# Kernel tuning notes

Measured on AMD Instinct MI355X. Metric: run time of the kernel, lower is better.

## Reference

```python
import jax, jax.numpy as jnp
import numpy as np

N_NODES = 100000
N_EDGES = 1600000
D_FEAT = 128
HIDDEN = 256


def setup_inputs() -> dict:
    key = jax.random.key(0)
    k1, k2, k3, k4, k5, k6, k7 = jax.random.split(key, 7)
    h = jax.random.normal(k1, (N_NODES, D_FEAT), dtype=jnp.float32)
    src = jax.random.randint(k2, (N_EDGES,), 0, N_NODES, dtype=jnp.int64)
    dst = jax.random.randint(k3, (N_EDGES,), 0, N_NODES, dtype=jnp.int64)
    # Linear weights, torch layout: W [out, in], b [out]
    lim1 = 1.0 / np.sqrt(2 * D_FEAT)
    W1_w = jax.random.uniform(k4, (HIDDEN, 2 * D_FEAT), minval=-lim1, maxval=lim1, dtype=jnp.float32)
    W1_b = jax.random.uniform(k5, (HIDDEN,), minval=-lim1, maxval=lim1, dtype=jnp.float32)
    lim2 = 1.0 / np.sqrt(HIDDEN)
    W2_w = jax.random.uniform(k6, (1, HIDDEN), minval=-lim2, maxval=lim2, dtype=jnp.float32)
    W2_b = jax.random.uniform(k7, (1,), minval=-lim2, maxval=lim2, dtype=jnp.float32)
    return {"h": h, "src": src, "dst": dst, "W1_w": W1_w, "W1_b": W1_b, "W2_w": W2_w, "W2_b": W2_b}


def reference(h, src, dst, W1_w, W1_b, W2_w, W2_b):
    # gather per-edge src/dst node features and concat: [E, 2D]
    x = jnp.concatenate([h[src], h[dst]], axis=1)
    # Linear -> ReLU -> Linear, squeeze last dim -> [E]
    hid = jax.nn.relu(x @ W1_w.T + W1_b)          # [E, H]
    score = (hid @ W2_w.T + W2_b)[:, 0]           # [E]
    return score
```

## Files before the change

### kernel.cpp

```cpp
#include <hip/hip_runtime.h>


#define NNODES 100000
#define E_TOTAL 1600000
#define D 128
#define K2 256
#define H 256

typedef short bf16x8 __attribute__((ext_vector_type(8)));
typedef short bf16x4 __attribute__((ext_vector_type(4)));
typedef float f32x4 __attribute__((ext_vector_type(4)));
typedef const __attribute__((address_space(1))) unsigned short* gas_t;
typedef __attribute__((address_space(3))) unsigned short* las_t;

__device__ __forceinline__ unsigned short f2bf(float f) {
    unsigned u = __float_as_uint(f);
    u += 0x7fff + ((u >> 16) & 1);
    return (unsigned short)(u >> 16);
}
__device__ __forceinline__ float bf2f(unsigned short s) {
    return __uint_as_float((unsigned)s << 16);
}

__global__ void cvt_w1(const float* __restrict__ W1, unsigned short* __restrict__ w1bf, int n4) {
    int i = blockIdx.x * blockDim.x + threadIdx.x;
    if (i >= n4) return;
    float4 v = ((const float4*)W1)[i];
    ushort4 o;
    o.x = f2bf(v.x); o.y = f2bf(v.y); o.z = f2bf(v.z); o.w = f2bf(v.w);
    ((ushort4*)w1bf)[i] = o;
}

__global__ __launch_bounds__(256, 2) void u_gemm(
    const float* __restrict__ h,
    const unsigned short* __restrict__ w1bf,
    const float* __restrict__ b1,
    unsigned short* __restrict__ Us,
    unsigned short* __restrict__ Ud)
{
    __shared__ __align__(16) unsigned short A[64 * 136];
    __shared__ __align__(16) unsigned short S[64 * 268];

    const int tid = threadIdx.x;
    const int wave = tid >> 6;
    const int lane = tid & 63;
    const int l15 = lane & 15;
    const int quad = lane >> 4;

    const int tile = blockIdx.x >> 1;
    const int half = blockIdx.x & 1;
    const int r0 = tile * 64;
    int rows = NNODES - r0; if (rows > 64) rows = 64;
    const int koff = half * 128;
    unsigned short* U = half ? Ud : Us;

    bf16x8 B[4][4];
    float bias[4];
#pragma unroll
    for (int nt = 0; nt < 4; ++nt) {
        const int n = wave * 64 + nt * 16 + l15;
        bias[nt] = half ? 0.f : b1[n];
#pragma unroll
        for (int kit = 0; kit < 4; ++kit)
            B[kit][nt] = *(const bf16x8*)(w1bf + (size_t)n * K2 + koff + kit * 32 + quad * 8);
    }

    const float4* hf4 = (const float4*)(h + (size_t)r0 * D);
    const int lim = rows * 32;
#pragma unroll
    for (int i = 0; i < 8; ++i) {
        int j = tid + i * 256;
        if (j < lim) {
            float4 v = hf4[j];
            bf16x4 b;
            b[0] = (short)f2bf(v.x); b[1] = (short)f2bf(v.y);
            b[2] = (short)f2bf(v.z); b[3] = (short)f2bf(v.w);
            *(bf16x4*)&A[(j >> 5) * 136 + (j & 31) * 4] = b;
        }
    }
    __syncthreads();

    f32x4 acc[4][4];
    const f32x4 zero = {0.f, 0.f, 0.f, 0.f};
#pragma unroll
    for (int ms = 0; ms < 4; ++ms)
#pragma unroll
        for (int nt = 0; nt < 4; ++nt)
            acc[ms][nt] = zero;

#pragma unroll
    for (int kit = 0; kit < 4; ++kit) {
        bf16x8 a[4];
#pragma unroll
        for (int ms = 0; ms < 4; ++ms)
            a[ms] = *(const bf16x8*)&A[(ms * 16 + l15) * 136 + kit * 32 + quad * 8];
#pragma unroll
        for (int ms = 0; ms < 4; ++ms)
#pragma unroll
            for (int nt = 0; nt < 4; ++nt)
                acc[ms][nt] = __builtin_amdgcn_mfma_f32_16x16x32_bf16(
                    a[ms], B[kit][nt], acc[ms][nt], 0, 0, 0);
    }

#pragma unroll
    for (int ms = 0; ms < 4; ++ms)
#pragma unroll
        for (int r = 0; r < 4; ++r) {
            const int m = ms * 16 + quad * 4 + r;
#pragma unroll
            for (int nt = 0; nt < 4; ++nt)
                S[m * 268 + wave * 64 + nt * 16 + l15] =
                    f2bf(acc[ms][nt][r] + bias[nt]);
        }
    __syncthreads();

#pragma unroll
    for (int i = 0; i < 8; ++i) {
        const int j = i * 256 + tid;
        const int row = j >> 5;
        const int cc = j & 31;
        if (row < rows) {
            bf16x8 vv = *(const bf16x8*)&S[row * 268 + cc * 8];
            *(bf16x8*)(U + (size_t)(r0 + row) * H + cc * 8) = vv;
        }
    }
}

__global__ __launch_bounds__(256) void edge_score(
    const unsigned short* __restrict__ Us,
    const unsigned short* __restrict__ Ud,
    const int* __restrict__ srcE,
    const int* __restrict__ dstE,
    const float* __restrict__ w2,
    const float* __restrict__ b2p,
    float* __restrict__ out,
    int grp0, int ngrp)
{
    const int gt = blockIdx.x * 256 + threadIdx.x;
    const int l = gt & 15;
    const int q = gt >> 4;
    const int Q = (gridDim.x * 256) >> 4;

    float w2v[16];
#pragma unroll
    for (int j = 0; j < 16; ++j) w2v[j] = w2[l * 16 + j];
    const float b2 = *b2p;

    for (int g = grp0 + q; g < grp0 + ngrp; g += Q) {
        const int e0 = g * 4;
        const int4 s4 = *(const int4*)(srcE + e0);
        const int4 d4 = *(const int4*)(dstE + e0);
        const int sv[4] = {s4.x, s4.y, s4.z, s4.w};
        const int dv[4] = {d4.x, d4.y, d4.z, d4.w};

        bf16x8 u[4][2], v[4][2];
#pragma unroll
        for (int k = 0; k < 4; ++k) {
            const bf16x8* us = (const bf16x8*)(Us + (size_t)sv[k] * H + l * 16);
            const bf16x8* ud = (const bf16x8*)(Ud + (size_t)dv[k] * H + l * 16);
            u[k][0] = us[0]; u[k][1] = us[1];
            v[k][0] = ud[0]; v[k][1] = ud[1];
        }

        float4 res;
        float* resp = (float*)&res;
#pragma unroll
        for (int k = 0; k < 4; ++k) {
            float acc = 0.f;
#pragma unroll
            for (int j = 0; j < 8; ++j) {
                float hv = bf2f((unsigned short)u[k][0][j]) + bf2f((unsigned short)v[k][0][j]);
                acc = fmaf(fmaxf(hv, 0.f), w2v[j], acc);
            }
#pragma unroll
            for (int j = 0; j < 8; ++j) {
                float hv = bf2f((unsigned short)u[k][1][j]) + bf2f((unsigned short)v[k][1][j]);
                acc = fmaf(fmaxf(hv, 0.f), w2v[j + 8], acc);
            }
            acc += __shfl_xor(acc, 1, 16);
            acc += __shfl_xor(acc, 2, 16);
            acc += __shfl_xor(acc, 4, 16);
            acc += __shfl_xor(acc, 8, 16);
            resp[k] = acc + b2;
        }
        if (l == 0) *(float4*)(out + e0) = res;
    }
}


#define TILE_M 32
#define NTILES (E_TOTAL / TILE_M)
#define GRID 2500

#if defined(__has_attribute)
#if __has_attribute(amdgpu_waves_per_eu)
#define LB __launch_bounds__(256) __attribute__((amdgpu_waves_per_eu(2, 2)))
#else
#define LB __launch_bounds__(256, 2)
#endif
#else
#define LB __launch_bounds__(256, 2)
#endif

__global__ void cvt_kernel(const float* __restrict__ h, const float* __restrict__ w1,
                           unsigned short* __restrict__ hbf, unsigned short* __restrict__ w1bf,
                           int n4h, int n4w) {
    int i = blockIdx.x * blockDim.x + threadIdx.x;
    const float* s; unsigned short* d; int j;
    if (i < n4h) { s = h; d = hbf; j = i; }
    else if (i < n4h + n4w) { s = w1; d = w1bf; j = i - n4h; }
    else return;
    float4 v = ((const float4*)s)[j];
    ushort4 o;
    o.x = f2bf(v.x); o.y = f2bf(v.y); o.z = f2bf(v.z); o.w = f2bf(v.w);
    ((ushort4*)d)[j] = o;
}

__global__ LB void edge_mlp(
    const unsigned short* __restrict__ hbf,
    const int* __restrict__ srcE,
    const int* __restrict__ dstE,
    const unsigned short* __restrict__ w1bf,
    const float* __restrict__ b1,
    const float* __restrict__ w2,
    const float* __restrict__ b2p,
    float* __restrict__ out)
{
    __shared__ __align__(16) unsigned short X[2][TILE_M * K2];
    __shared__ float red[2][TILE_M][5];

    const int tid = threadIdx.x;
    const int wave = tid >> 6;
    const int lane = tid & 63;
    const int lane15 = lane & 15;
    const int quad = lane >> 4;

    bf16x8 B[8][4];
#pragma unroll
    for (int kit = 0; kit < 8; ++kit)
#pragma unroll
        for (int nt = 0; nt < 4; ++nt) {
            int n = wave * 64 + nt * 16 + lane15;
            int k = kit * 32 + quad * 8;
            B[kit][nt] = *(const bf16x8*)(w1bf + n * K2 + k);
        }

    float b1v[4], w2v[4];
#pragma unroll
    for (int nt = 0; nt < 4; ++nt) {
        int n = wave * 64 + nt * 16 + lane15;
        b1v[nt] = b1[n];
        w2v[nt] = w2[n];
    }
    const float b2 = *b2p;

    const int r_off = tid >> 5;
    const int c = (tid & 31) ^ (r_off & 7);
    const int half = c >> 4;
    const int fc = c & 15;
    const int* idx_base = half ? dstE : srcE;
    const int gshort = fc * 8;

    const int t0 = blockIdx.x;
    int inode[4];

#pragma unroll
    for (int it = 0; it < 4; ++it)
        inode[it] = idx_base[t0 * TILE_M + it * 8 + r_off];
#pragma unroll
    for (int it = 0; it < 4; ++it)
        __builtin_amdgcn_global_load_lds(
            (gas_t)(hbf + inode[it] * D + gshort),
            (las_t)(&X[0][0] + it * 2048 + wave * 512), 16, 0, 0);
    {
        const int t1 = t0 + GRID;
#pragma unroll
        for (int it = 0; it < 4; ++it)
            inode[it] = idx_base[t1 * TILE_M + it * 8 + r_off];
    }

    int buf = 0;
    int prev_eb = -1;

    for (int tile = t0; tile < NTILES; tile += GRID) {
        __syncthreads();

        const int nt1 = tile + GRID;
        if (nt1 < NTILES) {
            unsigned short* Xn = &X[buf ^ 1][0];
#pragma unroll
            for (int it = 0; it < 4; ++it)
                __builtin_amdgcn_global_load_lds(
                    (gas_t)(hbf + inode[it] * D + gshort),
                    (las_t)(Xn + it * 2048 + wave * 512), 16, 0, 0);
        }
        const int nt2 = tile + 2 * GRID;
        if (nt2 < NTILES) {
            const int eb2 = nt2 * TILE_M;
#pragma unroll
            for (int it = 0; it < 4; ++it)
                inode[it] = idx_base[eb2 + it * 8 + r_off];
        }
        if (prev_eb >= 0 && tid < TILE_M) {
            float s = b2;
#pragma unroll
            for (int w = 0; w < 4; ++w) s += red[buf ^ 1][tid][w];
            out[prev_eb + tid] = s;
        }

        const unsigned short* Xc = &X[buf][0];
        f32x4 acc[2][4];
        const f32x4 zero = {0.f, 0.f, 0.f, 0.f};
#pragma unroll
        for (int ms = 0; ms < 2; ++ms)
#pragma unroll
            for (int nt = 0; nt < 4; ++nt)
                acc[ms][nt] = zero;

#pragma unroll
        for (int kit = 0; kit < 8; ++kit) {
            const int p8 = (((kit * 4 + quad) ^ (lane15 & 7))) * 8;
            bf16x8 a[2];
#pragma unroll
            for (int ms = 0; ms < 2; ++ms)
                a[ms] = *(const bf16x8*)&Xc[(ms * 16 + lane15) * K2 + p8];
#pragma unroll
            for (int ms = 0; ms < 2; ++ms)
#pragma unroll
                for (int nt = 0; nt < 4; ++nt)
                    acc[ms][nt] = __builtin_amdgcn_mfma_f32_16x16x32_bf16(
                        a[ms], B[kit][nt], acc[ms][nt], 0, 0, 0);
        }

#pragma unroll
        for (int ms = 0; ms < 2; ++ms)
#pragma unroll
            for (int r = 0; r < 4; ++r) {
                float p = 0.f;
#pragma unroll
                for (int nt = 0; nt < 4; ++nt) {
                    float hv = acc[ms][nt][r] + b1v[nt];
                    p = fmaf(fmaxf(hv, 0.f), w2v[nt], p);
                }
                p += __shfl_xor(p, 1, 16);
                p += __shfl_xor(p, 2, 16);
                p += __shfl_xor(p, 4, 16);
                p += __shfl_xor(p, 8, 16);
                if (lane15 == 0) red[buf][ms * 16 + quad * 4 + r][wave] = p;
            }
        prev_eb = tile * TILE_M;
        buf ^= 1;
    }

    __syncthreads();
    if (prev_eb >= 0 && tid < TILE_M) {
        float s = b2;
#pragma unroll
        for (int w = 0; w < 4; ++w) s += red[buf ^ 1][tid][w];
        out[prev_eb + tid] = s;
    }
}


extern "C" void kernel_launch(void* const* d_in, const int* in_sizes, int n_in,
                              void* d_out, int out_size, void* d_ws, size_t ws_size,
                              hipStream_t stream) {
    const float* h    = (const float*)d_in[0];
    const int*   srcE = (const int*)d_in[1];
    const int*   dstE = (const int*)d_in[2];
    const float* W1   = (const float*)d_in[3];
    const float* b1   = (const float*)d_in[4];
    const float* w2   = (const float*)d_in[5];
    const float* b2   = (const float*)d_in[6];
    float* out = (float*)d_out;

    char* ws = (char*)d_ws;
    const size_t offUs   = 0;
    const size_t offUd   = 51200000;
    const size_t offW1bf = 102400000;
    const size_t need    = offW1bf + 131072;

    if (ws_size >= need) {
        unsigned short* Us   = (unsigned short*)(ws + offUs);
        unsigned short* Ud   = (unsigned short*)(ws + offUd);
        unsigned short* w1bf = (unsigned short*)(ws + offW1bf);

        cvt_w1<<<(H * K2 / 4 + 255) / 256, 256, 0, stream>>>(W1, w1bf, H * K2 / 4);
        u_gemm<<<2 * ((NNODES + 63) / 64), 256, 0, stream>>>(h, w1bf, b1, Us, Ud);

        const int NGRP = E_TOTAL / 4;
        const int HALF_G = NGRP / 2;
        edge_score<<<2048, 256, 0, stream>>>(Us, Ud, srcE, dstE, w2, b2, out, 0, HALF_G);
        edge_score<<<2048, 256, 0, stream>>>(Us, Ud, srcE, dstE, w2, b2, out, HALF_G, HALF_G);
    } else {
        unsigned short* hbf  = (unsigned short*)d_ws;
        unsigned short* w1bf = hbf + (size_t)NNODES * D;
        int n4h = NNODES * D / 4;
        int n4w = H * K2 / 4;
        int n4 = n4h + n4w;
        cvt_kernel<<<(n4 + 255) / 256, 256, 0, stream>>>(h, W1, hbf, w1bf, n4h, n4w);
        edge_mlp<<<GRID, 256, 0, stream>>>(hbf, srcE, dstE, w1bf, b1, w2, b2, out);
    }
}
```

Before: 371.6 us.

## Pre-convert h to bf16 and stage it via direct global-to-LDS swizzled loads

Node features are converted to bf16 once by a separate kernel. The node GEMM then streams those bf16 rows straight into LDS with global_load_lds, using an XOR-swizzled layout in place of the padded one, so it no longer loads fp32 and converts in registers. The edge scoring pass is split into four launches instead of two. In exchange this adds a full conversion pass over h and needs more workspace; if the workspace is too small, it falls back to the old fused edge MLP path.

```diff
diff --git a/kernel.cpp b/kernel.cpp
--- a/kernel.cpp
+++ b/kernel.cpp
@@ -20,6 +20,20 @@
 }
 __device__ __forceinline__ float bf2f(unsigned short s) {
     return __uint_as_float((unsigned)s << 16);
+}
+
+__global__ void cvt_kernel(const float* __restrict__ h, const float* __restrict__ w1,
+                           unsigned short* __restrict__ hbf, unsigned short* __restrict__ w1bf,
+                           int n4h, int n4w) {
+    int i = blockIdx.x * blockDim.x + threadIdx.x;
+    const float* s; unsigned short* d; int j;
+    if (i < n4h) { s = h; d = hbf; j = i; }
+    else if (i < n4h + n4w) { s = w1; d = w1bf; j = i - n4h; }
+    else return;
+    float4 v = ((const float4*)s)[j];
+    ushort4 o;
+    o.x = f2bf(v.x); o.y = f2bf(v.y); o.z = f2bf(v.z); o.w = f2bf(v.w);
+    ((ushort4*)d)[j] = o;
 }
 
 __global__ void cvt_w1(const float* __restrict__ W1, unsigned short* __restrict__ w1bf, int n4) {
@@ -31,14 +45,14 @@
     ((ushort4*)w1bf)[i] = o;
 }
 
-__global__ __launch_bounds__(256, 2) void u_gemm(
-    const float* __restrict__ h,
+__global__ __launch_bounds__(256, 2) void u_gemm2(
+    const unsigned short* __restrict__ hbf,
     const unsigned short* __restrict__ w1bf,
     const float* __restrict__ b1,
     unsigned short* __restrict__ Us,
     unsigned short* __restrict__ Ud)
 {
-    __shared__ __align__(16) unsigned short A[64 * 136];
+    __shared__ __align__(16) unsigned short A[64 * 128];
     __shared__ __align__(16) unsigned short S[64 * 268];
 
     const int tid = threadIdx.x;
@@ -54,6 +68,18 @@
     const int koff = half * 128;
     unsigned short* U = half ? Ud : Us;
 
+#pragma unroll
+    for (int it = 0; it < 4; ++it) {
+        const int s = it * 256 + tid;
+        const int r = s >> 4;
+        const int p = s & 15;
+        const int c = p ^ (r & 15);
+        if (r < rows)
+            __builtin_amdgcn_global_load_lds(
+                (gas_t)(hbf + (size_t)(r0 + r) * D + c * 8),
+                (las_t)(A + it * 2048 + wave * 512), 16, 0, 0);
+    }
+
     bf16x8 B[4][4];
     float bias[4];
 #pragma unroll
@@ -65,19 +91,6 @@
             B[kit][nt] = *(const bf16x8*)(w1bf + (size_t)n * K2 + koff + kit * 32 + quad * 8);
     }
 
-    const float4* hf4 = (const float4*)(h + (size_t)r0 * D);
-    const int lim = rows * 32;
-#pragma unroll
-    for (int i = 0; i < 8; ++i) {
-        int j = tid + i * 256;
-        if (j < lim) {
-            float4 v = hf4[j];
-            bf16x4 b;
-            b[0] = (short)f2bf(v.x); b[1] = (short)f2bf(v.y);
-            b[2] = (short)f2bf(v.z); b[3] = (short)f2bf(v.w);
-            *(bf16x4*)&A[(j >> 5) * 136 + (j & 31) * 4] = b;
-        }
-    }
     __syncthreads();
 
     f32x4 acc[4][4];
@@ -92,8 +105,11 @@
     for (int kit = 0; kit < 4; ++kit) {
         bf16x8 a[4];
 #pragma unroll
-        for (int ms = 0; ms < 4; ++ms)
-            a[ms] = *(const bf16x8*)&A[(ms * 16 + l15) * 136 + kit * 32 + quad * 8];
+        for (int ms = 0; ms < 4; ++ms) {
+            const int row = ms * 16 + l15;
+            const int p = (kit * 4 + quad) ^ l15;
+            a[ms] = *(const bf16x8*)&A[row * 128 + p * 8];
+        }
 #pragma unroll
         for (int ms = 0; ms < 4; ++ms)
 #pragma unroll
@@ -202,20 +218,6 @@
 #define LB __launch_bounds__(256, 2)
 #endif
 
-__global__ void cvt_kernel(const float* __restrict__ h, const float* __restrict__ w1,
-                           unsigned short* __restrict__ hbf, unsigned short* __restrict__ w1bf,
-                           int n4h, int n4w) {
-    int i = blockIdx.x * blockDim.x + threadIdx.x;
-    const float* s; unsigned short* d; int j;
-    if (i < n4h) { s = h; d = hbf; j = i; }
-    else if (i < n4h + n4w) { s = w1; d = w1bf; j = i - n4h; }
-    else return;
-    float4 v = ((const float4*)s)[j];
-    ushort4 o;
-    o.x = f2bf(v.x); o.y = f2bf(v.y); o.z = f2bf(v.z); o.w = f2bf(v.w);
-    ((ushort4*)d)[j] = o;
-}
-
 __global__ LB void edge_mlp(
     const unsigned short* __restrict__ hbf,
     const int* __restrict__ srcE,
@@ -377,28 +379,40 @@
     char* ws = (char*)d_ws;
     const size_t offUs   = 0;
     const size_t offUd   = 51200000;
-    const size_t offW1bf = 102400000;
-    const size_t need    = offW1bf + 131072;
-
-    if (ws_size >= need) {
+    const size_t offHbf  = 102400000;
+    const size_t offW1v2 = 128000000;
+    const size_t needV2  = offW1v2 + 131072;
+    const size_t offW1v1 = 102400000;
+    const size_t needV1  = offW1v1 + 131072;
+
+    const int NGRP = E_TOTAL / 4;
+
+    if (ws_size >= needV2) {
         unsigned short* Us   = (unsigned short*)(ws + offUs);
         unsigned short* Ud   = (unsigned short*)(ws + offUd);
-        unsigned short* w1bf = (unsigned short*)(ws + offW1bf);
-
-        cvt_w1<<<(H * K2 / 4 + 255) / 256, 256, 0, stream>>>(W1, w1bf, H * K2 / 4);
-        u_gemm<<<2 * ((NNODES + 63) / 64), 256, 0, stream>>>(h, w1bf, b1, Us, Ud);
-
-        const int NGRP = E_TOTAL / 4;
-        const int HALF_G = NGRP / 2;
-        edge_score<<<2048, 256, 0, stream>>>(Us, Ud, srcE, dstE, w2, b2, out, 0, HALF_G);
-        edge_score<<<2048, 256, 0, stream>>>(Us, Ud, srcE, dstE, w2, b2, out, HALF_G, HALF_G);
+        unsigned short* hbf  = (unsigned short*)(ws + offHbf);
+        unsigned short* w1bf = (unsigned short*)(ws + offW1v2);
+
+        int n4h = NNODES * D / 4, n4w = H * K2 / 4;
+        cvt_kernel<<<(n4h + n4w + 255) / 256, 256, 0, stream>>>(h, W1, hbf, w1bf, n4h, n4w);
+        u_gemm2<<<2 * ((NNODES + 63) / 64), 256, 0, stream>>>(hbf, w1bf, b1, Us, Ud);
+
+        const int C = NGRP / 4;
+        edge_score<<<2048, 256, 0, stream>>>(Us, Ud, srcE, dstE, w2, b2, out, 0 * C, C);
+        edge_score<<<2048, 256, 0, stream>>>(Us, Ud, srcE, dstE, w2, b2, out, 1 * C, C);
+        edge_score<<<2048, 256, 0, stream>>>(Us, Ud, srcE, dstE, w2, b2, out, 2 * C, C);
+        edge_score<<<2048, 256, 0, stream>>>(Us, Ud, srcE, dstE, w2, b2, out, 3 * C, C);
+    } else if (ws_size >= needV1) {
+        unsigned short* hbf  = (unsigned short*)d_ws;
+        unsigned short* w1bf = hbf + (size_t)NNODES * D;
+        int n4h = NNODES * D / 4, n4w = H * K2 / 4;
+        cvt_kernel<<<(n4h + n4w + 255) / 256, 256, 0, stream>>>(h, W1, hbf, w1bf, n4h, n4w);
+        edge_mlp<<<GRID, 256, 0, stream>>>(hbf, srcE, dstE, w1bf, b1, w2, b2, out);
     } else {
         unsigned short* hbf  = (unsigned short*)d_ws;
         unsigned short* w1bf = hbf + (size_t)NNODES * D;
-        int n4h = NNODES * D / 4;
-        int n4w = H * K2 / 4;
-        int n4 = n4h + n4w;
-        cvt_kernel<<<(n4 + 255) / 256, 256, 0, stream>>>(h, W1, hbf, w1bf, n4h, n4w);
+        int n4h = NNODES * D / 4, n4w = H * K2 / 4;
+        cvt_kernel<<<(n4h + n4w + 255) / 256, 256, 0, stream>>>(h, W1, hbf, w1bf, n4h, n4w);
         edge_mlp<<<GRID, 256, 0, stream>>>(hbf, srcE, dstE, w1bf, b1, w2, b2, out);
     }
 }
```

Result: no change. 367.9 us (-1.0%).
